# Kernel optimization log

Hardware: AMD Instinct MI355X
Metric: run time of the kernel (lower is better)

## Reference

```python
import jax, jax.numpy as jnp
import numpy as np

EOS = 1e-10
ALPHA = 0.5
TEMPERATURE = 1.0
BIAS = 0.0001
N_NODES = 8192
N_EDGES = 262144
INPUT_DIM = 512
HIDDEN = 128


def setup_inputs() -> dict:
    key = jax.random.key(0)
    ks = jax.random.split(key, 7)
    features = jax.random.normal(ks[0], (N_NODES, INPUT_DIM), dtype=jnp.float32)
    W_emb = jax.random.normal(ks[1], (HIDDEN, INPUT_DIM), dtype=jnp.float32) * (1.0 / np.sqrt(INPUT_DIM))
    b_emb = jax.random.normal(ks[2], (HIDDEN,), dtype=jnp.float32) * 0.01
    W_edge = jax.random.normal(ks[3], (1, 2 * HIDDEN), dtype=jnp.float32) * (1.0 / np.sqrt(2 * HIDDEN))
    b_edge = jax.random.normal(ks[4], (1,), dtype=jnp.float32) * 0.01
    noise = jax.random.uniform(ks[5], (N_EDGES,), dtype=jnp.float32)
    edges = jax.random.randint(ks[6], (2, N_EDGES), 0, N_NODES, dtype=jnp.int64 if jax.config.jax_enable_x64 else jnp.int32)
    return {"features": features, "W_emb": W_emb, "b_emb": b_emb,
            "W_edge": W_edge, "b_edge": b_edge, "noise": noise, "edges": edges}


def _sym_normalize(adj):
    # inv_sqrt_degree[:,None] * adj * inv_sqrt_degree[None,:]
    inv_sqrt_deg = 1.0 / (jnp.sqrt(adj.sum(axis=1)) + EOS)
    return adj * inv_sqrt_deg[:, None] * inv_sqrt_deg[None, :]


def reference(features, W_emb, b_emb, W_edge, b_edge, noise, edges):
    n = N_NODES
    # node embedding: single Linear + ReLU
    h = jax.nn.relu(features @ W_emb.T + b_emb)            # [N, H]
    e0, e1 = edges[0], edges[1]
    h0, h1 = h[e0], h[e1]                                   # [E, H] gathers
    Wa, Wb = W_edge[0, :HIDDEN], W_edge[0, HIDDEN:]
    s1 = h0 @ Wa + h1 @ Wb + b_edge[0]                       # edge_mlp(cat(h0,h1))
    s2 = h1 @ Wa + h0 @ Wb + b_edge[0]                       # edge_mlp(cat(h1,h0))
    raw = 0.5 * (s1 + s2)                                    # [E]
    # gumbel gate: eps = (bias-(1-bias))*rand + (1-bias)
    eps = (BIAS - (1.0 - BIAS)) * noise + (1.0 - BIAS)
    gate = (jnp.log(eps) - jnp.log1p(-eps) + raw) / TEMPERATURE
    weights_lp = jax.nn.sigmoid(gate)                        # [E]
    weights_hp = 1.0 - weights_lp
    eye = jnp.eye(n, dtype=features.dtype)
    # scatter edge weights to dense adjacency (assignment semantics, like torch adj[e0,e1]=w)
    adj_lp = jnp.zeros((n, n), dtype=features.dtype).at[e0, e1].set(weights_lp) + eye
    adj_lp = _sym_normalize(adj_lp)
    adj_hp = jnp.zeros((n, n), dtype=features.dtype).at[e0, e1].set(weights_hp) + eye
    adj_hp = _sym_normalize(adj_hp)
    mask = jnp.zeros((n, n), dtype=features.dtype).at[e0, e1].set(1.0)
    adj_hp = eye - adj_hp * mask * ALPHA
    return (adj_lp, adj_hp, weights_lp, weights_hp)
```

## Files before the change

kernel.cpp:

```cpp
#include <hip/hip_runtime.h>
#include <cstdint>
#include <cstddef>

#define N_NODES 8192
#define N_EDGES 262144
#define INPUT_DIM 512
#define HIDDEN 128
#define ALPHA 0.5f
#define EOS 1e-10f
#define BCAP 128
#define LDA 40

typedef float v4 __attribute__((ext_vector_type(4)));
typedef __attribute__((ext_vector_type(8))) short short8;
typedef __attribute__((ext_vector_type(4))) float floatx4;

__device__ inline unsigned short f2bf(float x) {
    unsigned u = __builtin_bit_cast(unsigned, x);
    return (unsigned short)((u + 0x7FFFu + ((u >> 16) & 1u)) >> 16);
}
__device__ inline unsigned pack2(float a, float b) {
    return (unsigned)f2bf(a) | ((unsigned)f2bf(b) << 16);
}

__global__ __launch_bounds__(128) void k1_g(
    const float* __restrict__ F, const float* __restrict__ W,
    const float* __restrict__ bemb, const float* __restrict__ Wedge,
    float* __restrict__ g, int* __restrict__ cnt)
{
    __shared__ unsigned short As[32 * LDA];
    __shared__ unsigned short Bs[128 * LDA];
    int tid = threadIdx.x;
    int gt = blockIdx.x * 128 + tid;
    if (gt < N_NODES) cnt[gt] = 0;

    int node0 = blockIdx.x * 32;
    int lane = tid & 63, wave = tid >> 6;
    int ml = lane & 15, q = lane >> 4;

    floatx4 acc[8];
#pragma unroll
    for (int f = 0; f < 8; f++) acc[f] = 0.f;

    for (int s = 0; s < 16; s++) {
        int d0 = s * 32;
#pragma unroll
        for (int j = 0; j < 2; j++) {
            int qi = j * 128 + tid;
            int row = qi >> 3, dq = (qi & 7) * 4;
            float4 v = *(const float4*)&F[(size_t)(node0 + row) * INPUT_DIM + d0 + dq];
            uint2 p; p.x = pack2(v.x, v.y); p.y = pack2(v.z, v.w);
            *(uint2*)&As[row * LDA + dq] = p;
        }
#pragma unroll
        for (int j = 0; j < 8; j++) {
            int qi = j * 128 + tid;
            int row = qi >> 3, dq = (qi & 7) * 4;
            float4 v = *(const float4*)&W[(size_t)row * INPUT_DIM + d0 + dq];
            uint2 p; p.x = pack2(v.x, v.y); p.y = pack2(v.z, v.w);
            *(uint2*)&Bs[row * LDA + dq] = p;
        }
        __syncthreads();
        short8 a = *(const short8*)&As[(wave * 16 + ml) * LDA + q * 8];
#pragma unroll
        for (int f = 0; f < 8; f++) {
            short8 b = *(const short8*)&Bs[(f * 16 + ml) * LDA + q * 8];
            acc[f] = __builtin_amdgcn_mfma_f32_16x16x32_bf16(a, b, acc[f], 0, 0, 0);
        }
        __syncthreads();
    }
    float s0 = 0.f, s1 = 0.f, s2 = 0.f, s3 = 0.f;
#pragma unroll
    for (int f = 0; f < 8; f++) {
        int n = f * 16 + ml;
        float u = Wedge[n] + Wedge[HIDDEN + n];
        float bb = bemb[n];
        float h0 = acc[f][0] + bb; s0 += (h0 > 0.f ? h0 : 0.f) * u;
        float h1 = acc[f][1] + bb; s1 += (h1 > 0.f ? h1 : 0.f) * u;
        float h2 = acc[f][2] + bb; s2 += (h2 > 0.f ? h2 : 0.f) * u;
        float h3 = acc[f][3] + bb; s3 += (h3 > 0.f ? h3 : 0.f) * u;
    }
#pragma unroll
    for (int m = 1; m < 16; m <<= 1) {
        s0 += __shfl_xor(s0, m, 64);
        s1 += __shfl_xor(s1, m, 64);
        s2 += __shfl_xor(s2, m, 64);
        s3 += __shfl_xor(s3, m, 64);
    }
    if (ml == 0) {
        int node = node0 + wave * 16 + q * 4;
        g[node + 0] = s0; g[node + 1] = s1; g[node + 2] = s2; g[node + 3] = s3;
    }
}

__global__ __launch_bounds__(256) void k_edge(
    const int* __restrict__ edges, const float* __restrict__ noise,
    const float* __restrict__ g, const float* __restrict__ bedge,
    float* __restrict__ wlp, float* __restrict__ whp,
    int* __restrict__ cnt, int* __restrict__ bucket)
{
    int i = blockIdx.x * 256 + threadIdx.x;
    int e0 = edges[i], e1 = edges[N_EDGES + i];
    float raw = 0.5f * (g[e0] + g[e1]) + bedge[0];
    float eps = -0.9998f * noise[i] + 0.9999f;
    float gate = logf(eps) - log1pf(-eps) + raw;
    float w = 1.f / (1.f + expf(-gate));
    wlp[i] = w;
    whp[i] = 1.f - w;
    int pos = atomicAdd(&cnt[e0], 1);
    if (pos < BCAP) bucket[e0 * BCAP + pos] = i;
}

__global__ __launch_bounds__(256) void k_deginv(
    const int* __restrict__ edges, const float* __restrict__ wlp,
    const float* __restrict__ whp, const int* __restrict__ cnt,
    int* __restrict__ bucket, float* __restrict__ inv_lp, float* __restrict__ inv_hp)
{
    __shared__ int cols[2][BCAP];
    __shared__ int eidx[2][BCAP];
    __shared__ float plp[4], php[4];
    int tid = threadIdx.x;
    int half = tid >> 7, lt = tid & 127;
    int r = blockIdx.x * 2 + half;
    int d = cnt[r]; if (d > BCAP) d = BCAP;
    int i = -1, c = -1;
    if (lt < d) {
        i = bucket[r * BCAP + lt];
        c = edges[N_EDGES + i];
        cols[half][lt] = c;
        eidx[half][lt] = i;
    }
    __syncthreads();
    float sl = 0.f, sh = 0.f;
    if (lt < d) {
        bool win = true;
        for (int j = 0; j < d; j++)
            if (cols[half][j] == c && eidx[half][j] > i) { win = false; break; }
        int packv = -1;
        if (win) { sl = wlp[i]; sh = whp[i]; packv = (c << 18) | i; }
        bucket[r * BCAP + lt] = packv;
    }
#pragma unroll
    for (int m = 1; m < 64; m <<= 1) {
        sl += __shfl_xor(sl, m, 64);
        sh += __shfl_xor(sh, m, 64);
    }
    int wv = tid >> 6;
    if ((tid & 63) == 0) { plp[wv] = sl; php[wv] = sh; }
    __syncthreads();
    if (lt == 0) {
        float l = plp[half * 2] + plp[half * 2 + 1];
        float h = php[half * 2] + php[half * 2 + 1];
        inv_lp[r] = 1.f / (sqrtf(l + 1.f) + EOS);
        inv_hp[r] = 1.f / (sqrtf(h + 1.f) + EOS);
    }
}

__global__ __launch_bounds__(256) void k_fill(
    const float* __restrict__ wlp, const float* __restrict__ whp,
    const int* __restrict__ cnt, const int* __restrict__ bucket,
    const float* __restrict__ inv_lp, const float* __restrict__ inv_hp,
    float* __restrict__ LP, float* __restrict__ HP)
{
    __shared__ float row[N_NODES];
    int b = blockIdx.x, m = b & 1, r = b >> 1, tid = threadIdx.x;
    v4* rv = (v4*)row;
#pragma unroll
    for (int i = 0; i < 8; i++) rv[tid + i * 256] = 0.f;

    int d = cnt[r]; if (d > BCAP) d = BCAP;
    const float* wsrc = m ? whp : wlp;
    const float* isrc = m ? inv_hp : inv_lp;
    float ir = isrc[r];
    int pv = -1;
    if (tid < d) pv = bucket[r * BCAP + tid];
    __syncthreads();
    if (tid == 0) row[r] = m ? 1.0f : ir * ir;
    __syncthreads();
    if (pv >= 0) {
        int c = pv >> 18, i = pv & 0x3FFFF;
        float w = wsrc[i], ic = isrc[c];
        float diag = (c == r) ? 1.f : 0.f;
        row[c] = m ? (diag - (w + diag) * ir * ic * ALPHA)
                   : ((w + diag) * ir * ic);
    }
    __syncthreads();
    v4* dst = (v4*)((m ? HP : LP) + (size_t)r * N_NODES);
#pragma unroll
    for (int i = 0; i < 8; i++)
        __builtin_nontemporal_store(rv[tid + i * 256], &dst[tid + i * 256]);
}

extern "C" void kernel_launch(void* const* d_in, const int* in_sizes, int n_in,
                              void* d_out, int out_size, void* d_ws, size_t ws_size,
                              hipStream_t stream) {
    const float* F     = (const float*)d_in[0];
    const float* W     = (const float*)d_in[1];
    const float* bemb  = (const float*)d_in[2];
    const float* Wedge = (const float*)d_in[3];
    const float* bedge = (const float*)d_in[4];
    const float* noise = (const float*)d_in[5];
    const int*   edges = (const int*)d_in[6];

    const size_t N2 = (size_t)N_NODES * N_NODES;
    float* out = (float*)d_out;
    float* LP  = out;
    float* HP  = out + N2;
    float* wlp = HP + N2;
    float* whp = wlp + N_EDGES;

    char* ws = (char*)d_ws;
    float* g      = (float*)(ws);
    int*   cnt    = (int*)  (ws + 32768);
    float* inv_lp = (float*)(ws + 65536);
    float* inv_hp = (float*)(ws + 98304);
    int*   bucket = (int*)  (ws + 131072);

    k1_g<<<256, 128, 0, stream>>>(F, W, bemb, Wedge, g, cnt);
    k_edge<<<N_EDGES / 256, 256, 0, stream>>>(edges, noise, g, bedge,
                                              wlp, whp, cnt, bucket);
    k_deginv<<<N_NODES / 2, 256, 0, stream>>>(edges, wlp, whp, cnt, bucket,
                                              inv_lp, inv_hp);
    k_fill<<<2 * N_NODES, 256, 0, stream>>>(wlp, whp, cnt, bucket,
                                            inv_lp, inv_hp, LP, HP);
}
```

Before: 648.4 us.

## Fill LP and HP rows in one block via bitmap, prefetch GEMM tiles in registers

The fill kernel now writes both the LP and HP rows for a node in a single block. Instead of zeroing a 32 KB shared row, it builds a bitmap of occupied columns and scans the few nonzero entries per 4-column chunk while streaming zero-or-value vectors straight to global memory. Edge weights are staged in per-row bucket value arrays, which removes the scattered reads of wlp and whp. The GEMM kernel uses 256 threads with register prefetch of the next K tile and a split across hidden columns. The cost is extra workspace, plus a linear scan over the bucket for every nonempty chunk.

Measured after the change: 614.9 us. 1.05x faster.

```diff
diff --git a/kernel.cpp b/kernel.cpp
--- a/kernel.cpp
+++ b/kernel.cpp
@@ -23,73 +23,90 @@
     return (unsigned)f2bf(a) | ((unsigned)f2bf(b) << 16);
 }
 
-__global__ __launch_bounds__(128) void k1_g(
+__global__ __launch_bounds__(256) void k1_g(
     const float* __restrict__ F, const float* __restrict__ W,
     const float* __restrict__ bemb, const float* __restrict__ Wedge,
     float* __restrict__ g, int* __restrict__ cnt)
 {
     __shared__ unsigned short As[32 * LDA];
     __shared__ unsigned short Bs[128 * LDA];
+    __shared__ float part[4][16];
     int tid = threadIdx.x;
-    int gt = blockIdx.x * 128 + tid;
+    int gt = blockIdx.x * 256 + tid;
     if (gt < N_NODES) cnt[gt] = 0;
 
     int node0 = blockIdx.x * 32;
     int lane = tid & 63, wave = tid >> 6;
     int ml = lane & 15, q = lane >> 4;
-
-    floatx4 acc[8];
-#pragma unroll
-    for (int f = 0; f < 8; f++) acc[f] = 0.f;
+    int strip = wave & 1, hq = wave >> 1;
+
+    int arow = tid >> 3, ac4 = (tid & 7) * 4;
+    const float* Fp = &F[(size_t)(node0 + arow) * INPUT_DIM + ac4];
+    const float* Wp = &W[(size_t)arow * INPUT_DIM + ac4];
+
+    float4 aR = *(const float4*)Fp;
+    float4 bR0 = *(const float4*)(Wp + (size_t)(0 * 32) * INPUT_DIM);
+    float4 bR1 = *(const float4*)(Wp + (size_t)(1 * 32) * INPUT_DIM);
+    float4 bR2 = *(const float4*)(Wp + (size_t)(2 * 32) * INPUT_DIM);
+    float4 bR3 = *(const float4*)(Wp + (size_t)(3 * 32) * INPUT_DIM);
+
+    floatx4 acc[4];
+#pragma unroll
+    for (int j = 0; j < 4; j++) acc[j] = 0.f;
 
     for (int s = 0; s < 16; s++) {
-        int d0 = s * 32;
-#pragma unroll
-        for (int j = 0; j < 2; j++) {
-            int qi = j * 128 + tid;
-            int row = qi >> 3, dq = (qi & 7) * 4;
-            float4 v = *(const float4*)&F[(size_t)(node0 + row) * INPUT_DIM + d0 + dq];
-            uint2 p; p.x = pack2(v.x, v.y); p.y = pack2(v.z, v.w);
-            *(uint2*)&As[row * LDA + dq] = p;
-        }
-#pragma unroll
-        for (int j = 0; j < 8; j++) {
-            int qi = j * 128 + tid;
-            int row = qi >> 3, dq = (qi & 7) * 4;
-            float4 v = *(const float4*)&W[(size_t)row * INPUT_DIM + d0 + dq];
-            uint2 p; p.x = pack2(v.x, v.y); p.y = pack2(v.z, v.w);
-            *(uint2*)&Bs[row * LDA + dq] = p;
-        }
+        { uint2 p; p.x = pack2(aR.x, aR.y); p.y = pack2(aR.z, aR.w);
+          *(uint2*)&As[arow * LDA + ac4] = p; }
+        { uint2 p; p.x = pack2(bR0.x, bR0.y); p.y = pack2(bR0.z, bR0.w);
+          *(uint2*)&Bs[(0 * 32 + arow) * LDA + ac4] = p; }
+        { uint2 p; p.x = pack2(bR1.x, bR1.y); p.y = pack2(bR1.z, bR1.w);
+          *(uint2*)&Bs[(1 * 32 + arow) * LDA + ac4] = p; }
+        { uint2 p; p.x = pack2(bR2.x, bR2.y); p.y = pack2(bR2.z, bR2.w);
+          *(uint2*)&Bs[(2 * 32 + arow) * LDA + ac4] = p; }
+        { uint2 p; p.x = pack2(bR3.x, bR3.y); p.y = pack2(bR3.z, bR3.w);
+          *(uint2*)&Bs[(3 * 32 + arow) * LDA + ac4] = p; }
         __syncthreads();
-        short8 a = *(const short8*)&As[(wave * 16 + ml) * LDA + q * 8];
-#pragma unroll
-        for (int f = 0; f < 8; f++) {
-            short8 b = *(const short8*)&Bs[(f * 16 + ml) * LDA + q * 8];
-            acc[f] = __builtin_amdgcn_mfma_f32_16x16x32_bf16(a, b, acc[f], 0, 0, 0);
+        if (s < 15) {
+            int off = (s + 1) * 32;
+            aR  = *(const float4*)(Fp + off);
+            bR0 = *(const float4*)(Wp + off + (size_t)(0 * 32) * INPUT_DIM);
+            bR1 = *(const float4*)(Wp + off + (size_t)(1 * 32) * INPUT_DIM);
+            bR2 = *(const float4*)(Wp + off + (size_t)(2 * 32) * INPUT_DIM);
+            bR3 = *(const float4*)(Wp + off + (size_t)(3 * 32) * INPUT_DIM);
+        }
+        short8 a = *(const short8*)&As[(strip * 16 + ml) * LDA + q * 8];
+#pragma unroll
+        for (int j = 0; j < 4; j++) {
+            short8 b = *(const short8*)&Bs[((hq * 4 + j) * 16 + ml) * LDA + q * 8];
+            acc[j] = __builtin_amdgcn_mfma_f32_16x16x32_bf16(a, b, acc[j], 0, 0, 0);
         }
         __syncthreads();
     }
-    float s0 = 0.f, s1 = 0.f, s2 = 0.f, s3 = 0.f;
-#pragma unroll
-    for (int f = 0; f < 8; f++) {
-        int n = f * 16 + ml;
-        float u = Wedge[n] + Wedge[HIDDEN + n];
-        float bb = bemb[n];
-        float h0 = acc[f][0] + bb; s0 += (h0 > 0.f ? h0 : 0.f) * u;
-        float h1 = acc[f][1] + bb; s1 += (h1 > 0.f ? h1 : 0.f) * u;
-        float h2 = acc[f][2] + bb; s2 += (h2 > 0.f ? h2 : 0.f) * u;
-        float h3 = acc[f][3] + bb; s3 += (h3 > 0.f ? h3 : 0.f) * u;
+    float sr[4] = {0.f, 0.f, 0.f, 0.f};
+#pragma unroll
+    for (int j = 0; j < 4; j++) {
+        int hcol = (hq * 4 + j) * 16 + ml;
+        float u = Wedge[hcol] + Wedge[HIDDEN + hcol];
+        float bb = bemb[hcol];
+#pragma unroll
+        for (int rg = 0; rg < 4; rg++) {
+            float h = acc[j][rg] + bb;
+            sr[rg] += (h > 0.f ? h : 0.f) * u;
+        }
     }
 #pragma unroll
     for (int m = 1; m < 16; m <<= 1) {
-        s0 += __shfl_xor(s0, m, 64);
-        s1 += __shfl_xor(s1, m, 64);
-        s2 += __shfl_xor(s2, m, 64);
-        s3 += __shfl_xor(s3, m, 64);
+#pragma unroll
+        for (int rg = 0; rg < 4; rg++) sr[rg] += __shfl_xor(sr[rg], m, 16);
     }
     if (ml == 0) {
-        int node = node0 + wave * 16 + q * 4;
-        g[node + 0] = s0; g[node + 1] = s1; g[node + 2] = s2; g[node + 3] = s3;
+#pragma unroll
+        for (int rg = 0; rg < 4; rg++) part[wave][q * 4 + rg] = sr[rg];
+    }
+    __syncthreads();
+    if (tid < 32) {
+        int st = tid >> 4, ni = tid & 15;
+        g[node0 + st * 16 + ni] = part[st][ni] + part[st + 2][ni];
     }
 }
 
@@ -114,7 +131,8 @@
 __global__ __launch_bounds__(256) void k_deginv(
     const int* __restrict__ edges, const float* __restrict__ wlp,
     const float* __restrict__ whp, const int* __restrict__ cnt,
-    int* __restrict__ bucket, float* __restrict__ inv_lp, float* __restrict__ inv_hp)
+    int* __restrict__ bucket, float* __restrict__ bval_lp, float* __restrict__ bval_hp,
+    float* __restrict__ inv_lp, float* __restrict__ inv_hp)
 {
     __shared__ int cols[2][BCAP];
     __shared__ int eidx[2][BCAP];
@@ -136,9 +154,14 @@
         bool win = true;
         for (int j = 0; j < d; j++)
             if (cols[half][j] == c && eidx[half][j] > i) { win = false; break; }
-        int packv = -1;
-        if (win) { sl = wlp[i]; sh = whp[i]; packv = (c << 18) | i; }
-        bucket[r * BCAP + lt] = packv;
+        if (win) {
+            sl = wlp[i]; sh = whp[i];
+            bucket[r * BCAP + lt] = c;
+            bval_lp[r * BCAP + lt] = sl;
+            bval_hp[r * BCAP + lt] = sh;
+        } else {
+            bucket[r * BCAP + lt] = -1;
+        }
     }
 #pragma unroll
     for (int m = 1; m < 64; m <<= 1) {
@@ -157,38 +180,65 @@
 }
 
 __global__ __launch_bounds__(256) void k_fill(
-    const float* __restrict__ wlp, const float* __restrict__ whp,
     const int* __restrict__ cnt, const int* __restrict__ bucket,
+    const float* __restrict__ bval_lp, const float* __restrict__ bval_hp,
     const float* __restrict__ inv_lp, const float* __restrict__ inv_hp,
     float* __restrict__ LP, float* __restrict__ HP)
 {
-    __shared__ float row[N_NODES];
-    int b = blockIdx.x, m = b & 1, r = b >> 1, tid = threadIdx.x;
-    v4* rv = (v4*)row;
-#pragma unroll
-    for (int i = 0; i < 8; i++) rv[tid + i * 256] = 0.f;
-
+    __shared__ unsigned bm[256];
+    __shared__ int   s_col[BCAP + 1];
+    __shared__ float s_vlp[BCAP + 1];
+    __shared__ float s_vhp[BCAP + 1];
+    __shared__ int   s_d;
+    int r = blockIdx.x, tid = threadIdx.x;
+    bm[tid] = 0;
     int d = cnt[r]; if (d > BCAP) d = BCAP;
-    const float* wsrc = m ? whp : wlp;
-    const float* isrc = m ? inv_hp : inv_lp;
-    float ir = isrc[r];
-    int pv = -1;
-    if (tid < d) pv = bucket[r * BCAP + tid];
-    __syncthreads();
-    if (tid == 0) row[r] = m ? 1.0f : ir * ir;
-    __syncthreads();
-    if (pv >= 0) {
-        int c = pv >> 18, i = pv & 0x3FFFF;
-        float w = wsrc[i], ic = isrc[c];
+    float irl = inv_lp[r], irh = inv_hp[r];
+    __syncthreads();
+    int c = -1;
+    if (tid < d) c = bucket[r * BCAP + tid];
+    if (tid < d) s_col[tid] = c;
+    if (c >= 0) {
+        float w_lp = bval_lp[r * BCAP + tid];
+        float w_hp = bval_hp[r * BCAP + tid];
+        float icl = inv_lp[c], ich = inv_hp[c];
         float diag = (c == r) ? 1.f : 0.f;
-        row[c] = m ? (diag - (w + diag) * ir * ic * ALPHA)
-                   : ((w + diag) * ir * ic);
-    }
-    __syncthreads();
-    v4* dst = (v4*)((m ? HP : LP) + (size_t)r * N_NODES);
-#pragma unroll
-    for (int i = 0; i < 8; i++)
-        __builtin_nontemporal_store(rv[tid + i * 256], &dst[tid + i * 256]);
+        s_vlp[tid] = (w_lp + diag) * irl * icl;
+        s_vhp[tid] = diag - (w_hp + diag) * irh * ich * ALPHA;
+        atomicOr(&bm[c >> 5], 1u << (c & 31));
+    }
+    __syncthreads();
+    if (tid == 0) {
+        int dd = d;
+        if (!((bm[r >> 5] >> (r & 31)) & 1u)) {
+            s_col[dd] = r; s_vlp[dd] = irl * irl; s_vhp[dd] = 1.0f;
+            bm[r >> 5] |= 1u << (r & 31);
+            dd++;
+        }
+        s_d = dd;
+    }
+    __syncthreads();
+    int dd = s_d;
+    float* LPr = LP + (size_t)r * N_NODES;
+    float* HPr = HP + (size_t)r * N_NODES;
+#pragma unroll
+    for (int i = 0; i < 8; i++) {
+        int ch = i * 256 + tid;
+        unsigned nib = (bm[ch >> 3] >> ((ch & 7) * 4)) & 0xFu;
+        v4 lp = 0.f, hp = 0.f;
+        if (nib) {
+            for (int e = 0; e < dd; e++) {
+                int cc = s_col[e];
+                if ((cc >> 2) == ch) {
+                    int sl = cc & 3;
+                    ((float*)&lp)[sl] = s_vlp[e];
+                    ((float*)&hp)[sl] = s_vhp[e];
+                }
+            }
+        }
+        __builtin_nontemporal_store(lp, (v4*)&LPr[ch * 4]);
+        __builtin_nontemporal_store(hp, (v4*)&HPr[ch * 4]);
+    }
 }
 
 extern "C" void kernel_launch(void* const* d_in, const int* in_sizes, int n_in,
@@ -210,17 +260,19 @@
     float* whp = wlp + N_EDGES;
 
     char* ws = (char*)d_ws;
-    float* g      = (float*)(ws);
-    int*   cnt    = (int*)  (ws + 32768);
-    float* inv_lp = (float*)(ws + 65536);
-    float* inv_hp = (float*)(ws + 98304);
-    int*   bucket = (int*)  (ws + 131072);
-
-    k1_g<<<256, 128, 0, stream>>>(F, W, bemb, Wedge, g, cnt);
+    float* g       = (float*)(ws);
+    int*   cnt     = (int*)  (ws + 32768);
+    float* inv_lp  = (float*)(ws + 65536);
+    float* inv_hp  = (float*)(ws + 98304);
+    int*   bucket  = (int*)  (ws + 131072);
+    float* bval_lp = (float*)(ws + 131072 + (size_t)N_NODES * BCAP * 4);
+    float* bval_hp = (float*)(ws + 131072 + 2 * (size_t)N_NODES * BCAP * 4);
+
+    k1_g<<<256, 256, 0, stream>>>(F, W, bemb, Wedge, g, cnt);
     k_edge<<<N_EDGES / 256, 256, 0, stream>>>(edges, noise, g, bedge,
                                               wlp, whp, cnt, bucket);
     k_deginv<<<N_NODES / 2, 256, 0, stream>>>(edges, wlp, whp, cnt, bucket,
-                                              inv_lp, inv_hp);
-    k_fill<<<2 * N_NODES, 256, 0, stream>>>(wlp, whp, cnt, bucket,
-                                            inv_lp, inv_hp, LP, HP);
-}
+                                              bval_lp, bval_hp, inv_lp, inv_hp);
+    k_fill<<<N_NODES, 256, 0, stream>>>(cnt, bucket, bval_lp, bval_hp,
+                                        inv_lp, inv_hp, LP, HP);
+}
```
